# Kernel tuning notes

Hardware: AMD Instinct MI355X
Metric: run time of the kernel (lower is better)

## Reference

```python
import jax, jax.numpy as jnp
import numpy as np

NEG_INF = -1.0e9  # masked_fill value used by the torch module
LN_EPS = 1e-6


def setup_inputs() -> dict:
    key = jax.random.key(0)
    ks = jax.random.split(key, 10)
    B, S, D = 4, 1024, 1024
    H, DK, DV = 16, 64, 64
    q = jax.random.normal(ks[0], (B, S, D), dtype=jnp.float32)
    k = jax.random.normal(ks[1], (B, S, D), dtype=jnp.float32)
    v = jax.random.normal(ks[2], (B, S, D), dtype=jnp.float32)
    mask = jax.random.randint(ks[3], (B, S, S), 0, 2, dtype=jnp.int32)
    sc = 1.0 / np.sqrt(D)
    wq = jax.random.normal(ks[4], (H, D, DK), dtype=jnp.float32) * sc  # per-head W_qs stacked
    wk = jax.random.normal(ks[5], (H, D, DK), dtype=jnp.float32) * sc
    wv = jax.random.normal(ks[6], (H, D, DV), dtype=jnp.float32) * sc
    fc_w = jax.random.normal(ks[7], (D, H * DV), dtype=jnp.float32) * (1.0 / np.sqrt(H * DV))  # torch Linear weight [out,in]
    ln_g = jnp.ones((D,), dtype=jnp.float32)
    ln_b = jnp.zeros((D,), dtype=jnp.float32)
    return {"q": q, "k": k, "v": v, "mask": mask, "wq": wq, "wk": wk,
            "wv": wv, "fc_w": fc_w, "ln_g": ln_g, "ln_b": ln_b}


def reference(q, k, v, mask, wq, wk, wv, fc_w, ln_g, ln_b):
    # Batched equivalent of the per-head Python loop (dropout in eval mode = identity).
    B, S, D = q.shape
    H, _, DK = wq.shape
    DV = wv.shape[-1]
    temperature = jnp.asarray(DK, q.dtype) ** 0.5
    residual = q
    qh = jnp.einsum('bqd,hdk->bhqk', q, wq)   # [B,H,Q,DK]
    kh = jnp.einsum('bsd,hdk->bhsk', k, wk)   # [B,H,K,DK]
    vh = jnp.einsum('bsd,hdv->bhsv', v, wv)   # [B,H,K,DV]
    attn = jnp.einsum('bhqe,bhke->bhqk', qh / temperature, kh)  # [B,H,Q,K]
    attn = jnp.where(mask[:, None, :, :] == 0, jnp.asarray(NEG_INF, attn.dtype), attn)
    attn = jax.nn.softmax(attn, axis=-1)
    heads = jnp.einsum('bhqk,bhkv->bhqv', attn, vh)             # [B,H,Q,DV]
    # concat heads along feature dim in head order (matches torch.cat of the loop outputs)
    concat = jnp.transpose(heads, (0, 2, 1, 3)).reshape(B, S, H * DV)
    out = concat @ fc_w.T                                        # fc, no bias
    out = out + residual
    mu = jnp.mean(out, axis=-1, keepdims=True)
    var = jnp.mean(jnp.square(out - mu), axis=-1, keepdims=True)
    out = (out - mu) / jnp.sqrt(var + LN_EPS) * ln_g + ln_b
    return out
```

## Files before the change

### kernel.cpp

```cpp
#include <hip/hip_runtime.h>
#include <hip/hip_bf16.h>

typedef __bf16 bf16x8 __attribute__((ext_vector_type(8)));
typedef __bf16 bf16x4 __attribute__((ext_vector_type(4)));
typedef __bf16 bf16x2 __attribute__((ext_vector_type(2)));
typedef float f32x4 __attribute__((ext_vector_type(4)));
typedef unsigned int u32x2 __attribute__((ext_vector_type(2)));

#define MFMA16(a, b, c) __builtin_amdgcn_mfma_f32_16x16x32_bf16(a, b, c, 0, 0, 0)

static constexpr int M_ = 4096;

__device__ __forceinline__ void gload_lds16(const void* g, void* l) {
  __builtin_amdgcn_global_load_lds((const __attribute__((address_space(1))) void*)g,
                                   (__attribute__((address_space(3))) void*)l, 16, 0, 0);
}

__device__ __forceinline__ float exp2_hw(float x) {
  float r;
  asm("v_exp_f32 %0, %1" : "=v"(r) : "v"(x));
  return r;
}

#define SWZ(rowv, c16) (((rowv) * 64) + (((c16) ^ ((rowv) & 7)) * 8))

__global__ __launch_bounds__(256) void prep(const float* __restrict__ q,
                                            const float* __restrict__ k,
                                            const float* __restrict__ v,
                                            const float* __restrict__ fc_w,
                                            const float* __restrict__ wq,
                                            const float* __restrict__ wk,
                                            const float* __restrict__ wv,
                                            const int* __restrict__ mask,
                                            __bf16* __restrict__ QKVBF,
                                            __bf16* __restrict__ WFC,
                                            __bf16* __restrict__ W3T,
                                            unsigned long long* __restrict__ bits) {
  __shared__ float tile[64][65];
  int bx = blockIdx.x;
  const int t = threadIdx.x;

  if (bx < 6144) {
    const int z = bx >> 11;
    const float* src = z == 0 ? q : (z == 1 ? k : v);
    __bf16* dst = QKVBF + (size_t)z * 4194304;
    int i = (bx & 2047) * 256 + t;
    const float4* p = (const float4*)src + (size_t)i * 2;
    float4 a = p[0], b = p[1];
    bf16x8 o;
    o[0] = (__bf16)a.x; o[1] = (__bf16)a.y; o[2] = (__bf16)a.z; o[3] = (__bf16)a.w;
    o[4] = (__bf16)b.x; o[5] = (__bf16)b.y; o[6] = (__bf16)b.z; o[7] = (__bf16)b.w;
    *((bf16x8*)dst + i) = o;
    return;
  }
  bx -= 6144;
  if (bx < 512) {
    int i = bx * 256 + t;
    const float4* p = (const float4*)fc_w + (size_t)i * 2;
    float4 a = p[0], b = p[1];
    bf16x8 o;
    o[0] = (__bf16)a.x; o[1] = (__bf16)a.y; o[2] = (__bf16)a.z; o[3] = (__bf16)a.w;
    o[4] = (__bf16)b.x; o[5] = (__bf16)b.y; o[6] = (__bf16)b.z; o[7] = (__bf16)b.w;
    *((bf16x8*)WFC + i) = o;
    return;
  }
  bx -= 512;
  if (bx < 768) {
    const int z = bx >> 8, rem = bx & 255;
    const float* w = z == 0 ? wq : (z == 1 ? wk : wv);
    const float scale = z == 0 ? 0.125f * 1.4426950408889634f : 1.0f;
    __bf16* o = W3T + (size_t)z * 1048576;
    const int h = rem & 15, d0 = (rem >> 4) * 64;
    const int r = t >> 2, c0 = (t & 3) * 16;
    const float4* s4 = (const float4*)(w + ((size_t)h * 1024 + d0 + r) * 64 + c0);
#pragma unroll
    for (int j = 0; j < 4; ++j) {
      float4 vv = s4[j];
      tile[r][c0 + 4 * j + 0] = vv.x; tile[r][c0 + 4 * j + 1] = vv.y;
      tile[r][c0 + 4 * j + 2] = vv.z; tile[r][c0 + 4 * j + 3] = vv.w;
    }
    __syncthreads();
    __bf16* dst = o + ((size_t)(h * 64 + r)) * 1024 + d0 + c0;
    bf16x8 o0, o1;
#pragma unroll
    for (int j = 0; j < 8; ++j) o0[j] = (__bf16)(tile[c0 + j][r] * scale);
#pragma unroll
    for (int j = 0; j < 8; ++j) o1[j] = (__bf16)(tile[c0 + 8 + j][r] * scale);
    *(bf16x8*)dst = o0;
    *(bf16x8*)(dst + 8) = o1;
    return;
  }
  bx -= 768;
  {
    const int wid = bx * 4 + (t >> 6);
    const int lane = t & 63;
#pragma unroll
    for (int i = 0; i < 16; ++i) {
      int widx = wid * 16 + i;
      int qrow = widx & 1023;
      int bkt = widx >> 10;
      int b = bkt >> 4, kt = bkt & 15;
      int mval = mask[((size_t)b * 1024 + qrow) * 1024 + kt * 64 + lane];
      unsigned long long bal = __ballot(mval != 0);
      if (lane == 0) bits[widx] = bal;
    }
  }
}

__global__ __launch_bounds__(256) void gemm_qkv(const __bf16* __restrict__ Abase,
                                                const __bf16* __restrict__ Btbase,
                                                __bf16* __restrict__ HEADS) {
  __shared__ __bf16 SMEM[16384];
  const int L = blockIdx.x;
  const int wl = (L & 7) * 96 + (L >> 3);
  const int bn = wl & 7;
  const int bmz = wl >> 3;
  const int bm = bmz & 31, z = bmz >> 5;
  const __bf16* A = Abase + (size_t)z * 4194304;
  const __bf16* Bt = Btbase + (size_t)z * 1048576;
  const int tid = threadIdx.x, lane = tid & 63;
  const int w = tid >> 6;
  const int wr = (w >> 1) * 64, wc = (w & 1) * 64;
  const int lr = lane & 15, lh = lane >> 4;

  const int o0 = tid * 16;
  const int row0 = o0 >> 6, cb = o0 & 63;
  const char* apA0 = (const char*)A + ((size_t)(bm * 128 + row0) * 1024) * 2 + cb;
  const char* apA1 = apA0 + 64 * 2048;
  const char* apB0 = (const char*)Bt + ((size_t)(bn * 128 + row0) * 1024) * 2 + cb;
  const char* apB1 = apB0 + 64 * 2048;
  char* smem = (char*)SMEM;

#define QSTAGE(buf)                                         \
  do {                                                      \
    char* dd = smem + (buf) * 16384;                        \
    gload_lds16(apA0, dd + o0);                             \
    gload_lds16(apA1, dd + 4096 + o0);                      \
    gload_lds16(apB0, dd + 8192 + o0);                      \
    gload_lds16(apB1, dd + 12288 + o0);                     \
    apA0 += 64; apA1 += 64; apB0 += 64; apB1 += 64;         \
  } while (0)

  f32x4 acc[4][4];
#pragma unroll
  for (int m = 0; m < 4; ++m)
#pragma unroll
    for (int n = 0; n < 4; ++n) {
      f32x4 zz = {0.f, 0.f, 0.f, 0.f};
      acc[m][n] = zz;
    }

  QSTAGE(0);
  __syncthreads();

  for (int kt = 0; kt < 32; ++kt) {
    const int cur = kt & 1;
    if (kt < 31) QSTAGE(cur ^ 1);
    const int abase = cur * 8192;
    bf16x8 af[4], bfr[4];
#pragma unroll
    for (int m = 0; m < 4; ++m)
      af[m] = *(const bf16x8*)&SMEM[abase + (wr + m * 16 + lr) * 32 + lh * 8];
#pragma unroll
    for (int n = 0; n < 4; ++n)
      bfr[n] = *(const bf16x8*)&SMEM[abase + 4096 + (wc + n * 16 + lr) * 32 + lh * 8];
    __builtin_amdgcn_s_setprio(1);
#pragma unroll
    for (int m = 0; m < 4; ++m)
#pragma unroll
      for (int n = 0; n < 4; ++n) acc[m][n] = MFMA16(af[m], bfr[n], acc[m][n]);
    __builtin_amdgcn_s_setprio(0);
    __syncthreads();
  }
#undef QSTAGE

  if (z == 2) {
    const int hl = w & 1;
    const size_t vtbase = 2ull * 4194304;
    const size_t bb = (size_t)(bm >> 3) * 16 + bn * 2;
    const int kkbase = (bm & 7) * 128;
#pragma unroll
    for (int p = 0; p < 2; ++p) {
      if (hl == p) {
#pragma unroll
        for (int m = 0; m < 4; ++m)
#pragma unroll
          for (int n = 0; n < 4; ++n) {
            const int dk = n * 16 + lr;
            const int s = wr + m * 16 + lh * 4;
            bf16x4 pv;
#pragma unroll
            for (int j = 0; j < 4; ++j) pv[j] = (__bf16)acc[m][n][j];
            *(bf16x4*)&SMEM[dk * 132 + s] = pv;
          }
      }
      __syncthreads();
      {
        const int dk = tid >> 2, sc = tid & 3;
        const __bf16* srcp = &SMEM[dk * 132 + sc * 32];
        __bf16* dstp = HEADS + vtbase + ((bb + p) * 64 + dk) * 1024 + kkbase + sc * 32;
#pragma unroll
        for (int u = 0; u < 8; ++u) *(bf16x4*)(dstp + u * 4) = *(const bf16x4*)(srcp + u * 4);
      }
      __syncthreads();
    }
    return;
  }

#pragma unroll
  for (int p = 0; p < 2; ++p) {
    if ((w >> 1) == p) {
#pragma unroll
      for (int m = 0; m < 4; ++m)
#pragma unroll
        for (int n = 0; n < 4; ++n)
#pragma unroll
          for (int reg = 0; reg < 4; ++reg)
            SMEM[(m * 16 + lh * 4 + reg) * 132 + wc + n * 16 + lr] = (__bf16)acc[m][n][reg];
    }
    __syncthreads();
    {
      const int rowl = tid >> 2, c0 = (tid & 3) * 32;
      const int row = bm * 128 + p * 64 + rowl;
      const int b = row >> 10, s = row & 1023;
      const int h = bn * 2 + (c0 >> 6), dk0 = c0 & 63;
      __bf16* dst = HEADS + (size_t)z * 4194304 + (((size_t)b * 16 + h) * 1024 + s) * 64 + dk0;
      const __bf16* srcp = &SMEM[rowl * 132 + c0];
#pragma unroll
      for (int u = 0; u < 8; ++u) *(bf16x4*)(dst + u * 4) = *(const bf16x4*)(srcp + u * 4);
    }
    __syncthreads();
  }
}

__global__ __launch_bounds__(256) void gemm_fc64(const __bf16* __restrict__ A,
                                                 const __bf16* __restrict__ Bt,
                                                 float* __restrict__ O,
                                                 const float* __restrict__ resid) {
  __shared__ __bf16 SMEM[12288];
  const int L = blockIdx.x;
  const int wl = (L & 7) * 64 + (L >> 3);
  const int bn = wl & 7, bm = wl >> 3;
  const int tid = threadIdx.x, lane = tid & 63;
  const int w = tid >> 6;
  const int wc = w * 32;
  const int lr = lane & 15, lh = lane >> 4;

  const int o0 = tid * 16;
  const int row0 = o0 >> 6, cb = o0 & 63;
  const char* apA = (const char*)A + ((size_t)(bm * 64 + row0) * 1024) * 2 + cb;
  const char* apB0 = (const char*)Bt + ((size_t)(bn * 128 + row0) * 1024) * 2 + cb;
  const char* apB1 = apB0 + 64 * 2048;
  char* smem = (char*)SMEM;

#define FSTAGE(buf)                                         \
  do {                                                      \
    gload_lds16(apA, smem + (buf) * 4096 + o0);             \
    char* dd = smem + 8192 + (buf) * 8192;                  \
    gload_lds16(apB0, dd + o0);                             \
    gload_lds16(apB1, dd + 4096 + o0);                      \
    apA += 64; apB0 += 64; apB1 += 64;                      \
  } while (0)

  f32x4 acc[4][2];
#pragma unroll
  for (int m = 0; m < 4; ++m)
#pragma unroll
    for (int n = 0; n < 2; ++n) {
      f32x4 z = {0.f, 0.f, 0.f, 0.f};
      acc[m][n] = z;
    }

  FSTAGE(0);
  __syncthreads();

  for (int kt = 0; kt < 32; ++kt) {
    const int cur = kt & 1;
    if (kt < 31) FSTAGE(cur ^ 1);
    const int ab = cur * 2048;
    const int bb = 4096 + cur * 4096;
    bf16x8 af[4], bfr[2];
#pragma unroll
    for (int m = 0; m < 4; ++m) af[m] = *(const bf16x8*)&SMEM[ab + (m * 16 + lr) * 32 + lh * 8];
#pragma unroll
    for (int n = 0; n < 2; ++n)
      bfr[n] = *(const bf16x8*)&SMEM[bb + (wc + n * 16 + lr) * 32 + lh * 8];
    __builtin_amdgcn_s_setprio(1);
#pragma unroll
    for (int m = 0; m < 4; ++m)
#pragma unroll
      for (int n = 0; n < 2; ++n) acc[m][n] = MFMA16(af[m], bfr[n], acc[m][n]);
    __builtin_amdgcn_s_setprio(0);
    __syncthreads();
  }
#undef FSTAGE

#pragma unroll
  for (int m = 0; m < 4; ++m)
#pragma unroll
    for (int n = 0; n < 2; ++n)
#pragma unroll
      for (int reg = 0; reg < 4; ++reg) {
        int row = bm * 64 + m * 16 + lh * 4 + reg;
        int col = bn * 128 + wc + n * 16 + lr;
        size_t idx = (size_t)row * 1024 + col;
        O[idx] = acc[m][n][reg] + resid[idx];
      }
}

__global__ __launch_bounds__(256, 4) void attn_kernel(const __bf16* __restrict__ HEADS,
                                                      const unsigned long long* __restrict__ m64,
                                                      __bf16* __restrict__ concat) {
  const __bf16* QH = HEADS;
  const __bf16* KH = HEADS + (size_t)M_ * 1024;
  const __bf16* VT = HEADS + (size_t)2 * M_ * 1024;
  __shared__ __bf16 Ks[2][2][32 * 64];
  __shared__ __bf16 Vs[2][2][64 * 32];
  __shared__ unsigned Psw[2][4][256];

  const int d = blockIdx.x;
  const int xcd = d & 7, j = d >> 3;
  const int grp = xcd * 8 + (j >> 4);
  const int qt = j & 15;
  const int h = grp & 15, b = grp >> 4;

  const int tid = threadIdx.x, lane = tid & 63, w = tid >> 6;
  const int lr = lane & 15, lh = lane >> 4;
  const size_t headoff = ((size_t)b * 16 + h) * 65536;
  const char* Kbase = (const char*)(KH + headoff);
  const char* Vbase = (const char*)(VT + headoff);

  const int krow = tid >> 3, kg = tid & 7;
  const int kgo = krow * 128 + ((kg ^ (krow & 7)) * 16);
  const int vrow = tid >> 2, vg = tid & 3;
  const int vgo = vrow * 2048 + ((vg ^ ((vrow >> 1) & 3)) * 16);
  const int ldsb = tid * 16;

  const char* kpA = Kbase + kgo;
  const char* kpB = Kbase + 65536 + kgo;
  const char* vpA = Vbase + vgo;
  const char* vpB = Vbase + 1024 + vgo;

#define STAGE(buf)                                          \
  do {                                                      \
    gload_lds16(kpA, (char*)Ks[buf][0] + ldsb);             \
    gload_lds16(kpB, (char*)Ks[buf][1] + ldsb);             \
    gload_lds16(vpA, (char*)Vs[buf][0] + ldsb);             \
    gload_lds16(vpB, (char*)Vs[buf][1] + ldsb);             \
    kpA += 4096; kpB += 4096; vpA += 64; vpB += 64;         \
  } while (0)

  const int qrow = qt * 64 + w * 16 + lr;
  bf16x8 qa[2];
  {
    const __bf16* qptr = QH + headoff + (size_t)qrow * 64 + lh * 8;
    qa[0] = *(const bf16x8*)qptr;
    qa[1] = *(const bf16x8*)(qptr + 32);
  }
  f32x4 oacc[4];
#pragma unroll
  for (int g = 0; g < 4; ++g) {
    f32x4 z = {0.f, 0.f, 0.f, 0.f};
    oacc[g] = z;
  }
  float lrun = 0.f;

  const unsigned long long* m64A = m64 + (size_t)b * 16384 + qrow;
  const unsigned long long* m64B = m64A + 8192;
  unsigned long long pairA = m64A[0], pairB = m64B[0];
  unsigned long long pairAn = 0, pairBn = 0;

  const int vcol = (lh ^ ((lr >> 1) & 3)) * 8;
  const int pread = lr * 32 + vcol;
  const int pG = (lr >> 1) & 3;
  int kread[2][2], vread[4];
#pragma unroll
  for (int n = 0; n < 2; ++n)
#pragma unroll
    for (int h2 = 0; h2 < 2; ++h2) kread[n][h2] = SWZ(n * 16 + lr, h2 * 4 + lh);
#pragma unroll
  for (int g = 0; g < 4; ++g) vread[g] = (g * 16 + lr) * 32 + vcol;

  STAGE(0);
  __syncthreads();

#pragma unroll 2
  for (int t = 0; t < 16; ++t) {
    const int cur = t & 1;
    if ((t & 1) == 0 && t < 14) {
      pairAn = m64A[((t >> 1) + 1) * 1024];
      pairBn = m64B[((t >> 1) + 1) * 1024];
    }
    const unsigned mwA = (t & 1) ? (unsigned)(pairA >> 32) : (unsigned)pairA;
    const unsigned mwB = (t & 1) ? (unsigned)(pairB >> 32) : (unsigned)pairB;
    if (t < 15) STAGE(cur ^ 1);

    f32x4 sA[2], sB[2];
#pragma unroll
    for (int n = 0; n < 2; ++n) {
      f32x4 z = {0.f, 0.f, 0.f, 0.f};
      sA[n] = z; sB[n] = z;
    }
    __builtin_amdgcn_s_setprio(1);
#pragma unroll
    for (int n = 0; n < 2; ++n)
#pragma unroll
      for (int h2 = 0; h2 < 2; ++h2) {
        bf16x8 kbA = *(const bf16x8*)&Ks[cur][0][kread[n][h2]];
        bf16x8 kbB = *(const bf16x8*)&Ks[cur][1][kread[n][h2]];
        sA[n] = MFMA16(kbA, qa[h2], sA[n]);
        sB[n] = MFMA16(kbB, qa[h2], sB[n]);
      }
    __builtin_amdgcn_s_setprio(0);

#pragma unroll
    for (int n = 0; n < 2; ++n)
#pragma unroll
      for (int r = 0; r < 4; ++r) {
        unsigned bit = (mwA >> (n * 16 + lh * 4 + r)) & 1u;
        float p = bit ? exp2_hw(sA[n][r]) : 0.0f;
        sA[n][r] = p;
        lrun += p;
      }
#pragma unroll
    for (int n = 0; n < 2; ++n)
#pragma unroll
      for (int r = 0; r < 4; ++r) {
        unsigned bit = (mwB >> (n * 16 + lh * 4 + r)) & 1u;
        float p = bit ? exp2_hw(sB[n][r]) : 0.0f;
        sB[n][r] = p;
        lrun += p;
      }

#pragma unroll
    for (int n = 0; n < 2; ++n) {
      bf16x2 p0, p1;
      p0[0] = (__bf16)sA[n][0]; p0[1] = (__bf16)sA[n][1];
      p1[0] = (__bf16)sA[n][2]; p1[1] = (__bf16)sA[n][3];
      int G = n * 2 + (lh >> 1);
      int addr = lr * 16 + ((G ^ pG) * 4) + (lh & 1) * 2;
      u32x2 wv;
      wv[0] = __builtin_bit_cast(unsigned, p0);
      wv[1] = __builtin_bit_cast(unsigned, p1);
      *(u32x2*)&Psw[0][w][addr] = wv;
    }
#pragma unroll
    for (int n = 0; n < 2; ++n) {
      bf16x2 p0, p1;
      p0[0] = (__bf16)sB[n][0]; p0[1] = (__bf16)sB[n][1];
      p1[0] = (__bf16)sB[n][2]; p1[1] = (__bf16)sB[n][3];
      int G = n * 2 + (lh >> 1);
      int addr = lr * 16 + ((G ^ pG) * 4) + (lh & 1) * 2;
      u32x2 wv;
      wv[0] = __builtin_bit_cast(unsigned, p0);
      wv[1] = __builtin_bit_cast(unsigned, p1);
      *(u32x2*)&Psw[1][w][addr] = wv;
    }
    bf16x8 paA = *(const bf16x8*)&((const __bf16*)Psw[0][w])[pread];
    bf16x8 paB = *(const bf16x8*)&((const __bf16*)Psw[1][w])[pread];

    __builtin_amdgcn_s_setprio(1);
#pragma unroll
    for (int g = 0; g < 4; ++g) {
      bf16x8 vbA = *(const bf16x8*)&Vs[cur][0][vread[g]];
      bf16x8 vbB = *(const bf16x8*)&Vs[cur][1][vread[g]];
      oacc[g] = MFMA16(paA, vbA, oacc[g]);
      oacc[g] = MFMA16(paB, vbB, oacc[g]);
    }
    __builtin_amdgcn_s_setprio(0);
    if (t & 1) { pairA = pairAn; pairB = pairBn; }
    __syncthreads();
  }
#undef STAGE

  lrun += __shfl_xor(lrun, 16, 64);
  lrun += __shfl_xor(lrun, 32, 64);
  const float linv = 1.0f / (lrun + 1e-30f);
  const int qg0 = qt * 64 + w * 16 + lh * 4;
#pragma unroll
  for (int r = 0; r < 4; ++r) {
    const float ir = __shfl(linv, (lane & 48) | (lh * 4 + r), 64);
#pragma unroll
    for (int g = 0; g < 4; ++g)
      concat[((size_t)b * 1024 + qg0 + r) * 1024 + h * 64 + g * 16 + lr] =
          (__bf16)(oacc[g][r] * ir);
  }
}

__global__ __launch_bounds__(256) void ln_kernel(const float* __restrict__ in,
                                                 const float* __restrict__ gam,
                                                 const float* __restrict__ bet,
                                                 float* __restrict__ out) {
  const int row = blockIdx.x, t = threadIdx.x;
  const float4* x4 = (const float4*)(in + (size_t)row * 1024);
  float4 v = x4[t];
  float s = v.x + v.y + v.z + v.w;
  float sq = v.x * v.x + v.y * v.y + v.z * v.z + v.w * v.w;
#pragma unroll
  for (int off = 1; off < 64; off <<= 1) {
    s += __shfl_xor(s, off, 64);
    sq += __shfl_xor(sq, off, 64);
  }
  __shared__ float red[8];
  const int w = t >> 6, lane = t & 63;
  if (lane == 0) { red[w] = s; red[4 + w] = sq; }
  __syncthreads();
  s = red[0] + red[1] + red[2] + red[3];
  sq = red[4] + red[5] + red[6] + red[7];
  const float mu = s * (1.0f / 1024.0f);
  const float var = sq * (1.0f / 1024.0f) - mu * mu;
  const float rstd = rsqrtf(var + 1e-6f);
  float4 g4 = ((const float4*)gam)[t];
  float4 b4 = ((const float4*)bet)[t];
  float4 o;
  o.x = (v.x - mu) * rstd * g4.x + b4.x;
  o.y = (v.y - mu) * rstd * g4.y + b4.y;
  o.z = (v.z - mu) * rstd * g4.z + b4.z;
  o.w = (v.w - mu) * rstd * g4.w + b4.w;
  ((float4*)(out + (size_t)row * 1024))[t] = o;
}

extern "C" void kernel_launch(void* const* d_in, const int* in_sizes, int n_in,
                              void* d_out, int out_size, void* d_ws, size_t ws_size,
                              hipStream_t stream) {
  (void)in_sizes; (void)n_in; (void)out_size; (void)ws_size;
  const float* q = (const float*)d_in[0];
  const float* k = (const float*)d_in[1];
  const float* v = (const float*)d_in[2];
  const int* mask = (const int*)d_in[3];
  const float* wq = (const float*)d_in[4];
  const float* wk = (const float*)d_in[5];
  const float* wv = (const float*)d_in[6];
  const float* fc_w = (const float*)d_in[7];
  const float* ln_g = (const float*)d_in[8];
  const float* ln_b = (const float*)d_in[9];
  float* out = (float*)d_out;

  __bf16* QKVBF = (__bf16*)d_ws;
  __bf16* W3T   = QKVBF + 3ull * 4194304;
  __bf16* WFC   = W3T + 3ull * 1048576;
  __bf16* HEADS = WFC + 1048576;
  __bf16* CONCAT = HEADS + 3ull * 4194304;
  float* OUT1 = (float*)(CONCAT + 4194304);
  unsigned long long* MASKB = (unsigned long long*)OUT1;

  prep<<<8448, 256, 0, stream>>>(q, k, v, fc_w, wq, wk, wv, mask, QKVBF, WFC, W3T, MASKB);
  gemm_qkv<<<768, 256, 0, stream>>>(QKVBF, W3T, HEADS);
  attn_kernel<<<1024, 256, 0, stream>>>(HEADS, MASKB, CONCAT);
  gemm_fc64<<<512, 256, 0, stream>>>(CONCAT, WFC, OUT1, q);
  ln_kernel<<<4096, 256, 0, stream>>>(OUT1, ln_g, ln_b, out);
}
```

Baseline: 119.7 us.

## Fuse fp32-to-bf16 activation conversion into QKV projection GEMM A-tile loads

```diff
diff --git a/kernel.cpp b/kernel.cpp
--- a/kernel.cpp
+++ b/kernel.cpp
@@ -22,17 +22,20 @@
   return r;
 }
 
+__device__ __forceinline__ bf16x8 cvt8(float4 x, float4 y) {
+  bf16x8 o;
+  o[0] = (__bf16)x.x; o[1] = (__bf16)x.y; o[2] = (__bf16)x.z; o[3] = (__bf16)x.w;
+  o[4] = (__bf16)y.x; o[5] = (__bf16)y.y; o[6] = (__bf16)y.z; o[7] = (__bf16)y.w;
+  return o;
+}
+
 #define SWZ(rowv, c16) (((rowv) * 64) + (((c16) ^ ((rowv) & 7)) * 8))
 
-__global__ __launch_bounds__(256) void prep(const float* __restrict__ q,
-                                            const float* __restrict__ k,
-                                            const float* __restrict__ v,
-                                            const float* __restrict__ fc_w,
+__global__ __launch_bounds__(256) void prep(const float* __restrict__ fc_w,
                                             const float* __restrict__ wq,
                                             const float* __restrict__ wk,
                                             const float* __restrict__ wv,
                                             const int* __restrict__ mask,
-                                            __bf16* __restrict__ QKVBF,
                                             __bf16* __restrict__ WFC,
                                             __bf16* __restrict__ W3T,
                                             unsigned long long* __restrict__ bits) {
@@ -40,28 +43,11 @@
   int bx = blockIdx.x;
   const int t = threadIdx.x;
 
-  if (bx < 6144) {
-    const int z = bx >> 11;
-    const float* src = z == 0 ? q : (z == 1 ? k : v);
-    __bf16* dst = QKVBF + (size_t)z * 4194304;
-    int i = (bx & 2047) * 256 + t;
-    const float4* p = (const float4*)src + (size_t)i * 2;
-    float4 a = p[0], b = p[1];
-    bf16x8 o;
-    o[0] = (__bf16)a.x; o[1] = (__bf16)a.y; o[2] = (__bf16)a.z; o[3] = (__bf16)a.w;
-    o[4] = (__bf16)b.x; o[5] = (__bf16)b.y; o[6] = (__bf16)b.z; o[7] = (__bf16)b.w;
-    *((bf16x8*)dst + i) = o;
-    return;
-  }
-  bx -= 6144;
   if (bx < 512) {
     int i = bx * 256 + t;
     const float4* p = (const float4*)fc_w + (size_t)i * 2;
     float4 a = p[0], b = p[1];
-    bf16x8 o;
-    o[0] = (__bf16)a.x; o[1] = (__bf16)a.y; o[2] = (__bf16)a.z; o[3] = (__bf16)a.w;
-    o[4] = (__bf16)b.x; o[5] = (__bf16)b.y; o[6] = (__bf16)b.z; o[7] = (__bf16)b.w;
-    *((bf16x8*)WFC + i) = o;
+    *((bf16x8*)WFC + i) = cvt8(a, b);
     return;
   }
   bx -= 512;
@@ -107,7 +93,9 @@
   }
 }
 
-__global__ __launch_bounds__(256) void gemm_qkv(const __bf16* __restrict__ Abase,
+__global__ __launch_bounds__(256) void gemm_qkv(const float* __restrict__ q,
+                                                const float* __restrict__ k,
+                                                const float* __restrict__ v,
                                                 const __bf16* __restrict__ Btbase,
                                                 __bf16* __restrict__ HEADS) {
   __shared__ __bf16 SMEM[16384];
@@ -116,29 +104,28 @@
   const int bn = wl & 7;
   const int bmz = wl >> 3;
   const int bm = bmz & 31, z = bmz >> 5;
-  const __bf16* A = Abase + (size_t)z * 4194304;
+  const float* Af = z == 0 ? q : (z == 1 ? k : v);
   const __bf16* Bt = Btbase + (size_t)z * 1048576;
   const int tid = threadIdx.x, lane = tid & 63;
   const int w = tid >> 6;
   const int wr = (w >> 1) * 64, wc = (w & 1) * 64;
   const int lr = lane & 15, lh = lane >> 4;
 
+  const int rowA = tid >> 2, colf = (tid & 3) * 8;
+  const float* gA0 = Af + (size_t)(bm * 128 + rowA) * 1024 + colf;
+  const float* gA1 = gA0 + 64 * 1024;
   const int o0 = tid * 16;
   const int row0 = o0 >> 6, cb = o0 & 63;
-  const char* apA0 = (const char*)A + ((size_t)(bm * 128 + row0) * 1024) * 2 + cb;
-  const char* apA1 = apA0 + 64 * 2048;
   const char* apB0 = (const char*)Bt + ((size_t)(bn * 128 + row0) * 1024) * 2 + cb;
   const char* apB1 = apB0 + 64 * 2048;
-  char* smem = (char*)SMEM;
-
-#define QSTAGE(buf)                                         \
+  char* smemB = (char*)SMEM + 16384;
+
+#define BSTAGE(buf)                                         \
   do {                                                      \
-    char* dd = smem + (buf) * 16384;                        \
-    gload_lds16(apA0, dd + o0);                             \
-    gload_lds16(apA1, dd + 4096 + o0);                      \
-    gload_lds16(apB0, dd + 8192 + o0);                      \
-    gload_lds16(apB1, dd + 12288 + o0);                     \
-    apA0 += 64; apA1 += 64; apB0 += 64; apB1 += 64;         \
+    char* dd = smemB + (buf) * 8192;                        \
+    gload_lds16(apB0, dd + o0);                             \
+    gload_lds16(apB1, dd + 4096 + o0);                      \
+    apB0 += 64; apB1 += 64;                                 \
   } while (0)
 
   f32x4 acc[4][4];
@@ -150,34 +137,53 @@
       acc[m][n] = zz;
     }
 
-  QSTAGE(0);
+  {
+    float4 a0 = *(const float4*)gA0, a1 = *(const float4*)(gA0 + 4);
+    float4 b0 = *(const float4*)gA1, b1 = *(const float4*)(gA1 + 4);
+    gA0 += 32; gA1 += 32;
+    *(bf16x8*)((char*)SMEM + o0) = cvt8(a0, a1);
+    *(bf16x8*)((char*)SMEM + 4096 + o0) = cvt8(b0, b1);
+  }
+  BSTAGE(0);
   __syncthreads();
 
   for (int kt = 0; kt < 32; ++kt) {
     const int cur = kt & 1;
-    if (kt < 31) QSTAGE(cur ^ 1);
-    const int abase = cur * 8192;
+    float4 a0, a1, b0, b1;
+    if (kt < 31) {
+      a0 = *(const float4*)gA0; a1 = *(const float4*)(gA0 + 4);
+      b0 = *(const float4*)gA1; b1 = *(const float4*)(gA1 + 4);
+      gA0 += 32; gA1 += 32;
+      BSTAGE(cur ^ 1);
+    }
+    const int ab = cur * 4096;
+    const int bb = 8192 + cur * 4096;
     bf16x8 af[4], bfr[4];
 #pragma unroll
     for (int m = 0; m < 4; ++m)
-      af[m] = *(const bf16x8*)&SMEM[abase + (wr + m * 16 + lr) * 32 + lh * 8];
+      af[m] = *(const bf16x8*)&SMEM[ab + (wr + m * 16 + lr) * 32 + lh * 8];
 #pragma unroll
     for (int n = 0; n < 4; ++n)
-      bfr[n] = *(const bf16x8*)&SMEM[abase + 4096 + (wc + n * 16 + lr) * 32 + lh * 8];
+      bfr[n] = *(const bf16x8*)&SMEM[bb + (wc + n * 16 + lr) * 32 + lh * 8];
     __builtin_amdgcn_s_setprio(1);
 #pragma unroll
     for (int m = 0; m < 4; ++m)
 #pragma unroll
       for (int n = 0; n < 4; ++n) acc[m][n] = MFMA16(af[m], bfr[n], acc[m][n]);
     __builtin_amdgcn_s_setprio(0);
+    if (kt < 31) {
+      char* dA = (char*)SMEM + (cur ^ 1) * 8192;
+      *(bf16x8*)(dA + o0) = cvt8(a0, a1);
+      *(bf16x8*)(dA + 4096 + o0) = cvt8(b0, b1);
+    }
     __syncthreads();
   }
-#undef QSTAGE
+#undef BSTAGE
 
   if (z == 2) {
     const int hl = w & 1;
     const size_t vtbase = 2ull * 4194304;
-    const size_t bb = (size_t)(bm >> 3) * 16 + bn * 2;
+    const size_t bb2 = (size_t)(bm >> 3) * 16 + bn * 2;
     const int kkbase = (bm & 7) * 128;
 #pragma unroll
     for (int p = 0; p < 2; ++p) {
@@ -198,7 +204,7 @@
       {
         const int dk = tid >> 2, sc = tid & 3;
         const __bf16* srcp = &SMEM[dk * 132 + sc * 32];
-        __bf16* dstp = HEADS + vtbase + ((bb + p) * 64 + dk) * 1024 + kkbase + sc * 32;
+        __bf16* dstp = HEADS + vtbase + ((bb2 + p) * 64 + dk) * 1024 + kkbase + sc * 32;
 #pragma unroll
         for (int u = 0; u < 8; ++u) *(bf16x4*)(dstp + u * 4) = *(const bf16x4*)(srcp + u * 4);
       }
@@ -544,8 +550,8 @@
   float* OUT1 = (float*)(CONCAT + 4194304);
   unsigned long long* MASKB = (unsigned long long*)OUT1;
 
-  prep<<<8448, 256, 0, stream>>>(q, k, v, fc_w, wq, wk, wv, mask, QKVBF, WFC, W3T, MASKB);
-  gemm_qkv<<<768, 256, 0, stream>>>(QKVBF, W3T, HEADS);
+  prep<<<2304, 256, 0, stream>>>(fc_w, wq, wk, wv, mask, WFC, W3T, MASKB);
+  gemm_qkv<<<768, 256, 0, stream>>>(q, k, v, W3T, HEADS);
   attn_kernel<<<1024, 256, 0, stream>>>(HEADS, MASKB, CONCAT);
   gemm_fc64<<<512, 256, 0, stream>>>(CONCAT, WFC, OUT1, q);
   ln_kernel<<<4096, 256, 0, stream>>>(OUT1, ln_g, ln_b, out);
```

After: 113.1 us. -5.6%, faster.
